# Performance work log

Measured on AMD Instinct MI355X. Metric: run time of the kernel, lower is better.

Reference implementation:

```python
import jax, jax.numpy as jnp
import numpy as np

INDEX_SHIFT = jnp.array([[0, 0], [-1, 0], [1, 0], [0, 1], [-1, 1], [1, 1], [0, -1], [-1, -1], [1, -1]], dtype=jnp.int32)
GRID = jnp.array([513, 513], dtype=jnp.int32)  # pseudo_image_dims + 1


def setup_inputs() -> dict:
    key = jax.random.key(0)
    k1, k2, k3, k4 = jax.random.split(key, 4)
    li_bev_coors = jax.random.randint(k1, (8192, 2), 0, 512, dtype=jnp.int32)
    ra_bev_coors = jax.random.randint(k2, (2048, 2), 0, 512, dtype=jnp.int32)
    ra_pts = jax.random.normal(k3, (2048, 5), dtype=jnp.float32)
    ra_voxel_coords = jax.random.randint(k4, (2048, 3), 0, 512, dtype=jnp.int32)
    return {"li_bev_coors": li_bev_coors, "ra_bev_coors": ra_bev_coors,
            "ra_pts": ra_pts, "ra_voxel_coords": ra_voxel_coords}


def _neighbour_coors(bev_grids):
    # [N,2] -> [N,9,2]: shift by 9-neighborhood, wrap by (grid_size+1)
    return (bev_grids[:, None, :] + INDEX_SHIFT[None, :, :]) % GRID


def _nearest_dy(neighbour_coor, dy_coor, dy_mask):
    # neighbour_coor: [N,9,2] int; dy_coor: [M,2] float; dy_mask: [M] bool
    n = neighbour_coor.shape[0]
    a = neighbour_coor.reshape(-1, 2).astype(jnp.float32)        # [N*9, 2]
    a2 = jnp.sum(a * a, axis=-1)                                  # [N*9]
    b2 = jnp.sum(dy_coor * dy_coor, axis=-1)                      # [M]
    # squared euclidean distances (exact: integer coordinates)
    d2 = a2[:, None] + b2[None, :] - 2.0 * (a @ dy_coor.T)        # [N*9, M]
    d2 = jnp.where(dy_mask[None, :], d2, jnp.inf)                 # mask non-dynamic voxels
    dmin = jnp.sqrt(jnp.maximum(jnp.min(d2, axis=-1), 0.0))       # min commutes with sqrt
    return (dmin * 0.01).reshape(n, 9)


def reference(li_bev_coors, ra_bev_coors, ra_pts, ra_voxel_coords):
    # dynamic-point selection: |velocity| > 0.1 (column 4)
    dy_mask = jnp.abs(ra_pts[:, 4]) > 0.1                         # [M]
    dy_coor = ra_voxel_coords[:, 1:].astype(jnp.float32)          # [M,2]
    # (uniquifying dy_coor does not change the min-distance; skip for jit shapes)
    li_nb = _neighbour_coors(li_bev_coors)                        # [N_li,9,2]
    ra_nb = _neighbour_coors(ra_bev_coors)                        # [N_ra,9,2]
    use = jnp.sum(dy_mask) > 1
    li_dis = jnp.where(use, _nearest_dy(li_nb, dy_coor, dy_mask), 0.0)
    ra_dis = jnp.where(use, _nearest_dy(ra_nb, dy_coor, dy_mask), 0.0)
    return (li_dis, ra_dis)
```

## Files before the change

### kernel.cpp

```cpp
#include <hip/hip_runtime.h>

#define BLOCK 192
#define MAXM  2048


__device__ __forceinline__ float2 pk_fma2(float2 a, float2 b, float2 c) {
    return make_float2(fmaf(a.x, b.x, c.x), fmaf(a.y, b.y, c.y));
}

__global__ __launch_bounds__(BLOCK) void gauss_kernel(
    const int* __restrict__ li_coors, int n_li,
    const int* __restrict__ ra_coors, int n_ra,
    const float* __restrict__ pts,
    const int* __restrict__ vox,
    int m,
    float* __restrict__ out, int total)
{
    __shared__ __align__(16) float sx[MAXM];
    __shared__ __align__(16) float sy[MAXM];
    __shared__ __align__(16) float sc[MAXM];
    __shared__ int s_cnt;

    if (threadIdx.x == 0) s_cnt = 0;

    const int q = blockIdx.x * BLOCK + threadIdx.x;
    const bool valid = q < total;
    float nx = 0.0f, ny = 0.0f, q2 = 0.0f;
    if (valid) {
        const int shift_x[9] = {0,-1,1,0,-1,1,0,-1,1};
        const int shift_y[9] = {0, 0,0,1, 1,1,-1,-1,-1};
        const int li_total = n_li * 9;
        int n, s;
        const int* src;
        if (q < li_total) { n = q / 9; s = q - n * 9; src = li_coors; }
        else { int r = q - li_total; n = r / 9; s = r - n * 9; src = ra_coors; }
        int cx = src[n * 2 + 0] + shift_x[s];
        int cy = src[n * 2 + 1] + shift_y[s];
        if (cx < 0) cx += 513;
        if (cy < 0) cy += 513;
        float qx = (float)cx, qy = (float)cy;
        nx = -2.0f * qx;
        ny = -2.0f * qy;
        q2 = fmaf(qx, qx, qy * qy);
    }

    float mn = 3.4e38f;
    int nv = 0;

    for (int base = 0; base < m; base += MAXM) {
        const int cs = min(m - base, MAXM);
        const int csPad = (cs + 3) & ~3;

        __syncthreads();
        for (int i = threadIdx.x; i < csPad; i += BLOCK) {
            int gi = base + i;
            float x = 3.0e4f, y = 3.0e4f;
            if (i < cs && fabsf(pts[gi * 5 + 4]) > 0.1f) {
                ++nv;
                x = (float)vox[gi * 3 + 1];
                y = (float)vox[gi * 3 + 2];
            }
            sx[i] = x;
            sy[i] = y;
            sc[i] = fmaf(x, x, y * y);
        }
        __syncthreads();

        const float4* __restrict__ X4 = (const float4*)sx;
        const float4* __restrict__ Y4 = (const float4*)sy;
        const float4* __restrict__ C4 = (const float4*)sc;
        const float2 nx2 = make_float2(nx, nx);
        const float2 ny2 = make_float2(ny, ny);
        const int iters = csPad >> 2;
#pragma unroll 4
        for (int i = 0; i < iters; ++i) {
            float4 X = X4[i];
            float4 Y = Y4[i];
            float4 C = C4[i];
            float2 T01 = pk_fma2(make_float2(X.x, X.y), nx2,
                          pk_fma2(make_float2(Y.x, Y.y), ny2,
                                  make_float2(C.x, C.y)));
            float2 T23 = pk_fma2(make_float2(X.z, X.w), nx2,
                          pk_fma2(make_float2(Y.z, Y.w), ny2,
                                  make_float2(C.z, C.w)));
            mn = fminf(fminf(T01.x, T01.y), mn);
            mn = fminf(fminf(T23.x, T23.y), mn);
        }
    }

    if (nv) atomicAdd(&s_cnt, nv);
    __syncthreads();
    const int g = s_cnt;

    if (valid)
        out[q] = (g > 1) ? sqrtf(fmaxf(q2 + mn, 0.0f)) * 0.01f : 0.0f;
}

extern "C" void kernel_launch(void* const* d_in, const int* in_sizes, int n_in,
                              void* d_out, int out_size, void* d_ws, size_t ws_size,
                              hipStream_t stream) {
    const int*   li  = (const int*)d_in[0];
    const int*   ra  = (const int*)d_in[1];
    const float* pts = (const float*)d_in[2];
    const int*   vox = (const int*)d_in[3];

    const int n_li = in_sizes[0] / 2;
    const int n_ra = in_sizes[1] / 2;
    const int m    = in_sizes[2] / 5;

    const int total  = (n_li + n_ra) * 9;
    const int blocks = (total + BLOCK - 1) / BLOCK;

    gauss_kernel<<<blocks, BLOCK, 0, stream>>>(
        li, n_li, ra, n_ra, pts, vox, m, (float*)d_out, total);
}
```

Measured before the change: 88.52 us.

## Register-tile eight queries per thread and split candidates across waves

Each thread now holds eight query points in registers, so every pair of shared-memory candidate loads is reused across eight queries. The candidate set is split across sixteen waves, and the per-wave minima are combined through a shared-memory reduction. The precomputed squared-norm array is dropped and recomputed per candidate. The dynamic count now uses a wave ballot plus popcount. The aim is to cut LDS traffic per FMA, in exchange for far fewer blocks (about 180), more registers, and a final reduction step.

```diff
diff --git a/kernel.cpp b/kernel.cpp
--- a/kernel.cpp
+++ b/kernel.cpp
@@ -1,11 +1,17 @@
 #include <hip/hip_runtime.h>
 
-#define BLOCK 192
+#define NW    16
+#define BLOCK (NW * 64)
+#define QPT   8
+#define QPB   (64 * QPT)
 #define MAXM  2048
 
 
 __device__ __forceinline__ float2 pk_fma2(float2 a, float2 b, float2 c) {
     return make_float2(fmaf(a.x, b.x, c.x), fmaf(a.y, b.y, c.y));
+}
+__device__ __forceinline__ float2 pk_mul2(float2 a, float2 b) {
+    return make_float2(a.x * b.x, a.y * b.y);
 }
 
 __global__ __launch_bounds__(BLOCK) void gauss_kernel(
@@ -18,82 +24,108 @@
 {
     __shared__ __align__(16) float sx[MAXM];
     __shared__ __align__(16) float sy[MAXM];
-    __shared__ __align__(16) float sc[MAXM];
+    __shared__ __align__(16) float part[NW * QPB];
+    __shared__ float q2s[QPB];
     __shared__ int s_cnt;
 
-    if (threadIdx.x == 0) s_cnt = 0;
+    const int tid  = threadIdx.x;
+    const int lane = tid & 63;
+    const int w    = tid >> 6;
 
-    const int q = blockIdx.x * BLOCK + threadIdx.x;
-    const bool valid = q < total;
-    float nx = 0.0f, ny = 0.0f, q2 = 0.0f;
-    if (valid) {
-        const int shift_x[9] = {0,-1,1,0,-1,1,0,-1,1};
-        const int shift_y[9] = {0, 0,0,1, 1,1,-1,-1,-1};
-        const int li_total = n_li * 9;
-        int n, s;
-        const int* src;
-        if (q < li_total) { n = q / 9; s = q - n * 9; src = li_coors; }
-        else { int r = q - li_total; n = r / 9; s = r - n * 9; src = ra_coors; }
-        int cx = src[n * 2 + 0] + shift_x[s];
-        int cy = src[n * 2 + 1] + shift_y[s];
-        if (cx < 0) cx += 513;
-        if (cy < 0) cy += 513;
-        float qx = (float)cx, qy = (float)cy;
-        nx = -2.0f * qx;
-        ny = -2.0f * qy;
-        q2 = fmaf(qx, qx, qy * qy);
+    if (tid == 0) s_cnt = 0;
+
+    const int qbase = blockIdx.x * QPB;
+    const int li_total = n_li * 9;
+    float nx[QPT], ny[QPT], q2[QPT], mn[QPT];
+#pragma unroll
+    for (int k = 0; k < QPT; ++k) {
+        int q = qbase + lane + 64 * k;
+        float qx = 0.0f, qy = 0.0f;
+        if (q < total) {
+            const int shift_x[9] = {0,-1,1,0,-1,1,0,-1,1};
+            const int shift_y[9] = {0, 0,0,1, 1,1,-1,-1,-1};
+            int n, s;
+            const int* src;
+            if (q < li_total) { n = q / 9; s = q - n * 9; src = li_coors; }
+            else { int r = q - li_total; n = r / 9; s = r - n * 9; src = ra_coors; }
+            int cx = src[n * 2 + 0] + shift_x[s];
+            int cy = src[n * 2 + 1] + shift_y[s];
+            if (cx < 0) cx += 513;
+            if (cy < 0) cy += 513;
+            qx = (float)cx; qy = (float)cy;
+        }
+        nx[k] = -2.0f * qx;
+        ny[k] = -2.0f * qy;
+        q2[k] = fmaf(qx, qx, qy * qy);
+        mn[k] = 3.4e38f;
     }
 
-    float mn = 3.4e38f;
-    int nv = 0;
-
     for (int base = 0; base < m; base += MAXM) {
-        const int cs = min(m - base, MAXM);
-        const int csPad = (cs + 3) & ~3;
+        const int cs  = min(m - base, MAXM);
+        int per = (cs + NW - 1) / NW;
+        per = (per + 3) & ~3;
+        const int tot = NW * per;
 
         __syncthreads();
-        for (int i = threadIdx.x; i < csPad; i += BLOCK) {
+        for (int i = tid; i < tot; i += BLOCK) {
             int gi = base + i;
             float x = 3.0e4f, y = 3.0e4f;
+            bool dyn = false;
             if (i < cs && fabsf(pts[gi * 5 + 4]) > 0.1f) {
-                ++nv;
+                dyn = true;
                 x = (float)vox[gi * 3 + 1];
                 y = (float)vox[gi * 3 + 2];
             }
             sx[i] = x;
             sy[i] = y;
-            sc[i] = fmaf(x, x, y * y);
+            unsigned long long b = __ballot(dyn);
+            if (lane == 0 && b) atomicAdd(&s_cnt, (int)__popcll(b));
         }
         __syncthreads();
 
-        const float4* __restrict__ X4 = (const float4*)sx;
-        const float4* __restrict__ Y4 = (const float4*)sy;
-        const float4* __restrict__ C4 = (const float4*)sc;
-        const float2 nx2 = make_float2(nx, nx);
-        const float2 ny2 = make_float2(ny, ny);
-        const int iters = csPad >> 2;
+        const float4* __restrict__ X4 = (const float4*)sx + ((w * per) >> 2);
+        const float4* __restrict__ Y4 = (const float4*)sy + ((w * per) >> 2);
+        const int iters = per >> 2;
 #pragma unroll 4
         for (int i = 0; i < iters; ++i) {
             float4 X = X4[i];
             float4 Y = Y4[i];
-            float4 C = C4[i];
-            float2 T01 = pk_fma2(make_float2(X.x, X.y), nx2,
-                          pk_fma2(make_float2(Y.x, Y.y), ny2,
-                                  make_float2(C.x, C.y)));
-            float2 T23 = pk_fma2(make_float2(X.z, X.w), nx2,
-                          pk_fma2(make_float2(Y.z, Y.w), ny2,
-                                  make_float2(C.z, C.w)));
-            mn = fminf(fminf(T01.x, T01.y), mn);
-            mn = fminf(fminf(T23.x, T23.y), mn);
+            float2 X01 = make_float2(X.x, X.y), X23 = make_float2(X.z, X.w);
+            float2 Y01 = make_float2(Y.x, Y.y), Y23 = make_float2(Y.z, Y.w);
+            float2 C01 = pk_fma2(X01, X01, pk_mul2(Y01, Y01));
+            float2 C23 = pk_fma2(X23, X23, pk_mul2(Y23, Y23));
+#pragma unroll
+            for (int k = 0; k < QPT; ++k) {
+                float2 nx2 = make_float2(nx[k], nx[k]);
+                float2 ny2 = make_float2(ny[k], ny[k]);
+                float2 T01 = pk_fma2(X01, nx2, pk_fma2(Y01, ny2, C01));
+                float2 T23 = pk_fma2(X23, nx2, pk_fma2(Y23, ny2, C23));
+                mn[k] = fminf(fminf(T01.x, T01.y), mn[k]);
+                mn[k] = fminf(fminf(T23.x, T23.y), mn[k]);
+            }
         }
     }
 
-    if (nv) atomicAdd(&s_cnt, nv);
+#pragma unroll
+    for (int k = 0; k < QPT; ++k)
+        part[w * QPB + lane + 64 * k] = mn[k];
+    if (w == 0) {
+#pragma unroll
+        for (int k = 0; k < QPT; ++k)
+            q2s[lane + 64 * k] = q2[k];
+    }
     __syncthreads();
-    const int g = s_cnt;
 
-    if (valid)
-        out[q] = (g > 1) ? sqrtf(fmaxf(q2 + mn, 0.0f)) * 0.01f : 0.0f;
+    if (tid < QPB) {
+        float v = 3.4e38f;
+#pragma unroll
+        for (int w2 = 0; w2 < NW; ++w2)
+            v = fminf(v, part[w2 * QPB + tid]);
+        int gq = qbase + tid;
+        if (gq < total)
+            out[gq] = (s_cnt > 1) ? sqrtf(fmaxf(q2s[tid] + v, 0.0f)) * 0.01f
+                                  : 0.0f;
+    }
 }
 
 extern "C" void kernel_launch(void* const* d_in, const int* in_sizes, int n_in,
@@ -109,7 +141,7 @@
     const int m    = in_sizes[2] / 5;
 
     const int total  = (n_li + n_ra) * 9;
-    const int blocks = (total + BLOCK - 1) / BLOCK;
+    const int blocks = (total + QPB - 1) / QPB;
 
     gauss_kernel<<<blocks, BLOCK, 0, stream>>>(
         li, n_li, ra, n_ra, pts, vox, m, (float*)d_out, total);
```

Result: faster. 75.24 us (-15.0%).
